# Performance work log

Measured on AMD Instinct MI355X. Metric: run time of the kernel, lower is better.

## Reference

```python
import jax, jax.numpy as jnp
import numpy as np

K = 8  # hardcoded knn_point(8, ...) in the original module


def setup_inputs() -> dict:
    key = jax.random.key(0)
    k1, k2, k3 = jax.random.split(key, 3)
    B, N, S, C = 8, 8192, 2048, 256
    return {
        "xyz": jax.random.normal(k1, (B, 3, N), dtype=jnp.float32),
        "sparse_xyz": jax.random.normal(k2, (B, 3, S), dtype=jnp.float32),
        "sparse_feat": jax.random.normal(k3, (B, C, S), dtype=jnp.float32),
    }


def reference(xyz, sparse_xyz, sparse_feat):
    # xyz: [B,3,N] dense query points; sparse_xyz: [B,3,S]; sparse_feat: [B,C,S]
    B, _, N = xyz.shape
    x = jnp.transpose(xyz, (0, 2, 1))          # [B,N,3]
    sx = jnp.transpose(sparse_xyz, (0, 2, 1))  # [B,S,3]
    sf = jnp.transpose(sparse_feat, (0, 2, 1)) # [B,S,C]

    sqr = (jnp.sum(x * x, axis=-1)[:, :, None]
           + jnp.sum(sx * sx, axis=-1)[:, None, :]
           - 2.0 * jnp.einsum('bnc,bsc->bns', x, sx))

    # K nearest neighbors (smallest distance) -> indices [B,N,K]
    _, idx = jax.lax.top_k(-sqr, K)

    bidx = jnp.arange(B)[:, None, None]
    g_xyz = sx[bidx, idx]                      # gather neighbor coords [B,N,K,3]
    diff = g_xyz - x[:, :, None, :]
    dist = jnp.maximum(jnp.linalg.norm(diff, axis=3), 1e-10)  # [B,N,K]

    inv = 1.0 / dist
    weight = inv / jnp.sum(inv, axis=2, keepdims=True)        # [B,N,K]

    g_feat = sf[bidx, idx]                     # gather neighbor feats [B,N,K,C]
    dense = jnp.sum(weight[..., None] * g_feat, axis=2)       # [B,N,C]
    return jnp.transpose(dense, (0, 2, 1))     # [B,C,N]
```

## Files before the change

### kernel.cpp

```cpp
#include <hip/hip_runtime.h>
#include <hip/hip_fp16.h>

#define BB 8
#define NN 8192
#define SS 2048
#define CC 256
#define KNN 8
#define TOPM 10
#define NLIST 4
#define QPB 64
#define MSTRIDE 41
#define FSTR 12

#define UMIN(a, b) __builtin_elementwise_min(a, b)
#define UMAX(a, b) __builtin_elementwise_max(a, b)
#define UMIN3(a, b, c) UMIN(UMIN(a, b), c)

typedef short bf16x8_t __attribute__((ext_vector_type(8)));
typedef float f32x4_t __attribute__((ext_vector_type(4)));

__device__ __forceinline__ unsigned pack_h2(float a, float b) {
    __half2 h = __halves2half2(__float2half_rn(a), __float2half_rn(b));
    return *reinterpret_cast<unsigned*>(&h);
}
__device__ __forceinline__ float2 unpack_h2(unsigned u) {
    __half2 h = *reinterpret_cast<__half2*>(&u);
    return __half22float2(h);
}

__device__ __forceinline__ unsigned short f2bf(float f) {
    unsigned u = __float_as_uint(f);
    u += 0x7FFFu + ((u >> 16) & 1u);
    return (unsigned short)(u >> 16);
}
__device__ __forceinline__ float bf2f(unsigned short h) {
    return __uint_as_float((unsigned)h << 16);
}

__device__ __forceinline__ void ins2(unsigned k1[TOPM], unsigned ca, unsigned cb) {
    unsigned lo = UMIN(ca, cb), hi = UMAX(ca, cb);
#pragma unroll
    for (int j = TOPM - 1; j >= 2; --j)
        k1[j] = UMIN3(k1[j], UMAX(k1[j - 1], lo), UMAX(k1[j - 2], hi));
    k1[1] = UMIN3(k1[1], UMAX(k1[0], lo), hi);
    k1[0] = UMIN(k1[0], lo);
}

__device__ __forceinline__ void ins_step(unsigned k1[TOPM], f32x4_t d, unsigned sbase) {
    unsigned c0 = (__float_as_uint(d[0]) & 0xFFFFF800u) | sbase;
    unsigned c1 = (__float_as_uint(d[1]) & 0xFFFFF800u) | (sbase + 1u);
    unsigned c2 = (__float_as_uint(d[2]) & 0xFFFFF800u) | (sbase + 2u);
    unsigned c3 = (__float_as_uint(d[3]) & 0xFFFFF800u) | (sbase + 3u);
    ins2(k1, c0, c1);
    ins2(k1, c2, c3);
}

__global__ __launch_bounds__(256) void prep_kernel(
    const float* __restrict__ sxyz,
    unsigned short* __restrict__ gt)
{
    const int b = blockIdx.x;
    const int tid = threadIdx.x;
    const float* sb = sxyz + (long)b * 3 * SS;
    unsigned short* gb = gt + (long)b * 2 * SS * 8;
#pragma unroll
    for (int i = 0; i < SS / 256; ++i) {
        int s = i * 256 + tid;
        float px = sb[s], py = sb[SS + s], pz = sb[2 * SS + s];
        unsigned short xh = f2bf(px); unsigned short xl = f2bf(px - bf2f(xh));
        unsigned short yh = f2bf(py); unsigned short yl = f2bf(py - bf2f(yh));
        unsigned short zh = f2bf(pz); unsigned short zl = f2bf(pz - bf2f(zh));
        float pn = fmaf(px, px, fmaf(py, py, pz * pz));
        unsigned short nh = f2bf(pn); unsigned short nl = f2bf(pn - bf2f(nh));
        const unsigned ONE = 0x3F80u;
        uint4 t0 = make_uint4((unsigned)xh | ((unsigned)xl << 16),
                              (unsigned)xh | ((unsigned)yh << 16),
                              (unsigned)yl | ((unsigned)yh << 16),
                              (unsigned)zh | ((unsigned)zl << 16));
        uint4 t1 = make_uint4((unsigned)zh | ((unsigned)nh << 16),
                              (unsigned)nl | (ONE << 16),
                              ONE, 0u);
        *(uint4*)&gb[(long)s * 8] = t0;
        *(uint4*)&gb[((long)SS + s) * 8] = t1;
    }
}

__global__ __launch_bounds__(256, 4) void knn_kernel(
    const float* __restrict__ xyz,
    const float* __restrict__ sxyz,
    const unsigned short* __restrict__ gt,
    unsigned* __restrict__ out_pk)
{
    __shared__ unsigned mbuf[QPB * MSTRIDE];

    const int b    = blockIdx.x >> 7;
    const int q0   = (blockIdx.x & 127) * QPB;
    const int tid  = threadIdx.x;
    const int wave = tid >> 6;
    const int lane = tid & 63;
    const int g    = lane >> 4;
    const int qi   = lane & 15;

    const float* sb = sxyz + (long)b * 3 * SS;
    const float* xb = xyz + (long)b * 3 * NN;

    const int nq = q0 + wave * 16 + qi;
    const float qx = xb[nq], qy = xb[NN + nq], qz = xb[2 * NN + nq];

    bf16x8_t qf = (bf16x8_t)0;
    {
        unsigned short xh = f2bf(qx); float xhf = bf2f(xh);
        unsigned short yh = f2bf(qy); float yhf = bf2f(yh);
        unsigned short zh = f2bf(qz); float zhf = bf2f(zh);
        unsigned short xh2 = f2bf(-2.f * xhf), xl2 = f2bf(-2.f * (qx - xhf));
        unsigned short yh2 = f2bf(-2.f * yhf), yl2 = f2bf(-2.f * (qy - yhf));
        unsigned short zh2 = f2bf(-2.f * zhf), zl2 = f2bf(-2.f * (qz - zhf));
        float qn = fmaf(qx, qx, fmaf(qy, qy, qz * qz)) + 0.0625f;
        unsigned short nh = f2bf(qn); unsigned short nl = f2bf(qn - bf2f(nh));
        const short ONE = (short)0x3F80;
        if (g == 0) {
            qf[0] = (short)xh2; qf[1] = (short)xh2; qf[2] = (short)xl2;
            qf[3] = (short)yh2; qf[4] = (short)yh2; qf[5] = (short)yl2;
            qf[6] = (short)zh2; qf[7] = (short)zh2;
        } else if (g == 1) {
            qf[0] = (short)zl2; qf[1] = ONE; qf[2] = ONE;
            qf[3] = (short)nh;  qf[4] = (short)nl;
        }
    }

    const unsigned short* abase =
        gt + (long)b * 2 * SS * 8 + (long)(g & 1) * SS * 8 + qi * 8;

    unsigned k1[TOPM];
#pragma unroll
    for (int j = 0; j < TOPM; ++j) k1[j] = 0xFFFFFFFFu;

    const f32x4_t zacc = {0.f, 0.f, 0.f, 0.f};
    const unsigned ib4 = (unsigned)(g * 4);

    bf16x8_t af = *(const bf16x8_t*)abase; abase += 128;
    f32x4_t dc = __builtin_amdgcn_mfma_f32_16x16x32_bf16(af, qf, zacc, 0, 0, 0);

#pragma unroll 2
    for (int step = 0; step < 127; ++step) {
        bf16x8_t an = *(const bf16x8_t*)abase; abase += 128;
        f32x4_t dn = __builtin_amdgcn_mfma_f32_16x16x32_bf16(an, qf, zacc, 0, 0, 0);
        ins_step(k1, dc, ib4 + (unsigned)(step * 16));
        dc = dn;
    }
    ins_step(k1, dc, ib4 + (unsigned)(127 * 16));

    {
        unsigned* m1 = &mbuf[(wave * 16 + qi) * MSTRIDE + g * TOPM];
#pragma unroll
        for (int j = 0; j < TOPM; ++j) m1[j] = k1[j];
    }
    __syncthreads();

    if (tid < QPB) {
        const int n2 = q0 + tid;
        const double dqx = (double)xb[n2], dqy = (double)xb[NN + n2], dqz = (double)xb[2 * NN + n2];
        const unsigned* ml = &mbuf[tid * MSTRIDE];

        unsigned long long top[KNN];
#pragma unroll
        for (int j = 0; j < KNN; ++j) top[j] = ~0ull;

#pragma unroll 4
        for (int j = 0; j < NLIST * TOPM; ++j) {
            unsigned key = ml[j];
            int s = key & 0x7FF;
            float px = sb[s], py = sb[SS + s], pz = sb[2 * SS + s];
            double ex = (double)px - dqx;
            double ey = (double)py - dqy;
            double ez = (double)pz - dqz;
            double dd = ex * ex + ey * ey + ez * ez;
            unsigned long long c =
                (((unsigned long long)__double_as_longlong(dd)) & ~0x7FFull) | (unsigned long long)s;
#pragma unroll
            for (int jj = KNN - 1; jj >= 1; --jj)
                top[jj] = UMIN(UMAX(top[jj - 1], c), top[jj]);
            top[0] = UMIN(top[0], c);
        }

        const float fqx = xb[n2], fqy = xb[NN + n2], fqz = xb[2 * NN + n2];
        int   id[KNN];
        float inv[KNN];
        float ssum = 0.f;
#pragma unroll
        for (int k = 0; k < KNN; ++k) {
            id[k] = (int)(top[k] & 0x7FFull);
            float px = sb[id[k]], py = sb[SS + id[k]], pz = sb[2 * SS + id[k]];
            float dx = px - fqx, dy = py - fqy, dz = pz - fqz;
            float dv = sqrtf(dx * dx + dy * dy + dz * dz);
            dv = fmaxf(dv, 1e-10f);
            inv[k] = 1.0f / dv;
            ssum += inv[k];
        }
        const float rs = 1.0f / ssum;
        const long base = ((long)b * NN + n2) * KNN;
#pragma unroll
        for (int k = 0; k < KNN; ++k) {
            unsigned hw = (unsigned)__half_as_ushort(__float2half_rn(inv[k] * rs));
            out_pk[base + k] = (hw << 16) | (unsigned)id[k];
        }
    }
}

__global__ __launch_bounds__(256, 2) void accum_kernel(
    const float*    __restrict__ sf,
    const unsigned* __restrict__ pk,
    float* __restrict__ out)
{
    __shared__ unsigned short feat[SS * FSTR];

    const int blk  = blockIdx.x;
    const int b    = blk >> 6;
    const int ct   = (blk >> 1) & 31;
    const int half = blk & 1;
    const int t    = threadIdx.x;
    const int c0   = ct * 8;

    const float* sfb = sf + ((long)b * CC + c0) * SS;
#pragma unroll
    for (int i = 0; i < SS / 256; ++i) {
        int s = i * 256 + t;
        float f[8];
#pragma unroll
        for (int c = 0; c < 8; ++c) f[c] = sfb[(long)c * SS + s];
        uint2 w0 = make_uint2(pack_h2(f[0], f[1]), pack_h2(f[2], f[3]));
        uint2 w1 = make_uint2(pack_h2(f[4], f[5]), pack_h2(f[6], f[7]));
        *(uint2*)&feat[s * FSTR]     = w0;
        *(uint2*)&feat[s * FSTR + 4] = w1;
    }
    __syncthreads();

    const unsigned* pkb = pk + ((long)b * NN + half * 4096) * KNN;
    float* outb = out + ((long)b * CC + c0) * NN + half * 4096;

    for (int it = 0; it < 4096 / 256; ++it) {
        const int nrel = it * 256 + t;
        const uint4 pa = *(const uint4*)(pkb + (long)nrel * KNN);
        const uint4 pb = *(const uint4*)(pkb + (long)nrel * KNN + 4);
        const unsigned pks[8] = {pa.x, pa.y, pa.z, pa.w, pb.x, pb.y, pb.z, pb.w};

        float acc[8];
#pragma unroll
        for (int c = 0; c < 8; ++c) acc[c] = 0.f;

#pragma unroll
        for (int k = 0; k < KNN; ++k) {
            const unsigned p = pks[k];
            const int id = p & 0x7FF;
            const float w = __half2float(__ushort_as_half((unsigned short)(p >> 16)));
            const unsigned short* fp = &feat[id * FSTR];
            uint2 A = *(const uint2*)fp;
            uint2 B = *(const uint2*)(fp + 4);
            float2 f0 = unpack_h2(A.x), f1 = unpack_h2(A.y);
            float2 f2 = unpack_h2(B.x), f3 = unpack_h2(B.y);
            acc[0] = fmaf(w, f0.x, acc[0]);
            acc[1] = fmaf(w, f0.y, acc[1]);
            acc[2] = fmaf(w, f1.x, acc[2]);
            acc[3] = fmaf(w, f1.y, acc[3]);
            acc[4] = fmaf(w, f2.x, acc[4]);
            acc[5] = fmaf(w, f2.y, acc[5]);
            acc[6] = fmaf(w, f3.x, acc[6]);
            acc[7] = fmaf(w, f3.y, acc[7]);
        }

#pragma unroll
        for (int c = 0; c < 8; ++c)
            outb[(long)c * NN + nrel] = acc[c];
    }
}

extern "C" void kernel_launch(void* const* d_in, const int* in_sizes, int n_in,
                              void* d_out, int out_size, void* d_ws, size_t ws_size,
                              hipStream_t stream) {
    const float* xyz  = (const float*)d_in[0];
    const float* sxyz = (const float*)d_in[1];
    const float* sf   = (const float*)d_in[2];
    float* out = (float*)d_out;

    unsigned* pkbuf = (unsigned*)d_ws;
    unsigned short* gtile = (unsigned short*)((char*)d_ws + (size_t)BB * NN * KNN * 4);

    prep_kernel<<<dim3(BB), dim3(256), 0, stream>>>(sxyz, gtile);
    knn_kernel<<<dim3(BB * NN / QPB), dim3(256), 0, stream>>>(xyz, sxyz, gtile, pkbuf);
    accum_kernel<<<dim3(BB * 32 * 2), dim3(256), 0, stream>>>(sf, pkbuf, out);
}
```

Baseline: 175.6 us.

## Fuse feature accumulation into knn kernel using pre-transposed fp16 features

Adds a prep kernel that transposes sparse features into an [B,S,C] fp16 layout. The weighted gather-accumulate is folded into the knn kernel: neighbor indices and weights stay in LDS, and each block reads 16-byte feature rows from global/L2 instead of staging 8-channel slices in LDS. This drops the packed-index workspace round trip and the separate accum launch. In exchange, feature gathers become scattered global reads. Output stores also become strided, with four threads per query writing channels NN apart, so store coalescing worsens.

Result: slower. 179.3 us (+2.1%).

```diff
diff --git a/kernel.cpp b/kernel.cpp
--- a/kernel.cpp
+++ b/kernel.cpp
@@ -10,7 +10,7 @@
 #define NLIST 4
 #define QPB 64
 #define MSTRIDE 41
-#define FSTR 12
+#define TSTR 264
 
 #define UMIN(a, b) __builtin_elementwise_min(a, b)
 #define UMAX(a, b) __builtin_elementwise_max(a, b)
@@ -19,10 +19,6 @@
 typedef short bf16x8_t __attribute__((ext_vector_type(8)));
 typedef float f32x4_t __attribute__((ext_vector_type(4)));
 
-__device__ __forceinline__ unsigned pack_h2(float a, float b) {
-    __half2 h = __halves2half2(__float2half_rn(a), __float2half_rn(b));
-    return *reinterpret_cast<unsigned*>(&h);
-}
 __device__ __forceinline__ float2 unpack_h2(unsigned u) {
     __half2 h = *reinterpret_cast<__half2*>(&u);
     return __half22float2(h);
@@ -85,13 +81,46 @@
     }
 }
 
+__global__ __launch_bounds__(256) void prep2_kernel(
+    const float* __restrict__ sf,
+    unsigned short* __restrict__ sft)
+{
+    __shared__ unsigned short ts[64 * TSTR];
+
+    const int blk = blockIdx.x;
+    const int b   = blk >> 5;
+    const int st  = blk & 31;
+    const int t   = threadIdx.x;
+
+    const int s  = t & 63;
+    const int cq = t >> 6;
+    const float* sfb = sf + (long)b * CC * SS + (long)st * 64;
+#pragma unroll
+    for (int it = 0; it < CC / 4; ++it) {
+        int c = it * 4 + cq;
+        float v = sfb[(long)c * SS + s];
+        ts[s * TSTR + c] = __half_as_ushort(__float2half_rn(v));
+    }
+    __syncthreads();
+
+    const int so = t >> 2;
+    const int co = (t & 3) * 64;
+    unsigned short* dst = sft + ((long)b * SS + st * 64 + so) * CC + co;
+    const unsigned short* src = &ts[so * TSTR + co];
+#pragma unroll
+    for (int i = 0; i < 8; ++i)
+        *(uint4*)&dst[i * 8] = *(const uint4*)&src[i * 8];
+}
+
 __global__ __launch_bounds__(256, 4) void knn_kernel(
     const float* __restrict__ xyz,
     const float* __restrict__ sxyz,
     const unsigned short* __restrict__ gt,
-    unsigned* __restrict__ out_pk)
+    const unsigned short* __restrict__ sft,
+    float* __restrict__ out)
 {
     __shared__ unsigned mbuf[QPB * MSTRIDE];
+    __shared__ unsigned pk_lds[QPB * KNN];
 
     const int b    = blockIdx.x >> 7;
     const int q0   = (blockIdx.x & 127) * QPB;
@@ -128,7 +157,7 @@
         }
     }
 
-    const unsigned short* abase =
+    const unsigned short* ap =
         gt + (long)b * 2 * SS * 8 + (long)(g & 1) * SS * 8 + qi * 8;
 
     unsigned k1[TOPM];
@@ -138,12 +167,12 @@
     const f32x4_t zacc = {0.f, 0.f, 0.f, 0.f};
     const unsigned ib4 = (unsigned)(g * 4);
 
-    bf16x8_t af = *(const bf16x8_t*)abase; abase += 128;
+    bf16x8_t af = *(const bf16x8_t*)ap; ap += 128;
     f32x4_t dc = __builtin_amdgcn_mfma_f32_16x16x32_bf16(af, qf, zacc, 0, 0, 0);
 
 #pragma unroll 2
     for (int step = 0; step < 127; ++step) {
-        bf16x8_t an = *(const bf16x8_t*)abase; abase += 128;
+        bf16x8_t an = *(const bf16x8_t*)ap; ap += 128;
         f32x4_t dn = __builtin_amdgcn_mfma_f32_16x16x32_bf16(an, qf, zacc, 0, 0, 0);
         ins_step(k1, dc, ib4 + (unsigned)(step * 16));
         dc = dn;
@@ -198,79 +227,52 @@
             ssum += inv[k];
         }
         const float rs = 1.0f / ssum;
-        const long base = ((long)b * NN + n2) * KNN;
 #pragma unroll
         for (int k = 0; k < KNN; ++k) {
             unsigned hw = (unsigned)__half_as_ushort(__float2half_rn(inv[k] * rs));
-            out_pk[base + k] = (hw << 16) | (unsigned)id[k];
-        }
-    }
-}
-
-__global__ __launch_bounds__(256, 2) void accum_kernel(
-    const float*    __restrict__ sf,
-    const unsigned* __restrict__ pk,
-    float* __restrict__ out)
-{
-    __shared__ unsigned short feat[SS * FSTR];
-
-    const int blk  = blockIdx.x;
-    const int b    = blk >> 6;
-    const int ct   = (blk >> 1) & 31;
-    const int half = blk & 1;
-    const int t    = threadIdx.x;
-    const int c0   = ct * 8;
-
-    const float* sfb = sf + ((long)b * CC + c0) * SS;
-#pragma unroll
-    for (int i = 0; i < SS / 256; ++i) {
-        int s = i * 256 + t;
-        float f[8];
-#pragma unroll
-        for (int c = 0; c < 8; ++c) f[c] = sfb[(long)c * SS + s];
-        uint2 w0 = make_uint2(pack_h2(f[0], f[1]), pack_h2(f[2], f[3]));
-        uint2 w1 = make_uint2(pack_h2(f[4], f[5]), pack_h2(f[6], f[7]));
-        *(uint2*)&feat[s * FSTR]     = w0;
-        *(uint2*)&feat[s * FSTR + 4] = w1;
+            pk_lds[tid * KNN + k] = (hw << 16) | (unsigned)id[k];
+        }
     }
     __syncthreads();
 
-    const unsigned* pkb = pk + ((long)b * NN + half * 4096) * KNN;
-    float* outb = out + ((long)b * CC + c0) * NN + half * 4096;
-
-    for (int it = 0; it < 4096 / 256; ++it) {
-        const int nrel = it * 256 + t;
-        const uint4 pa = *(const uint4*)(pkb + (long)nrel * KNN);
-        const uint4 pb = *(const uint4*)(pkb + (long)nrel * KNN + 4);
-        const unsigned pks[8] = {pa.x, pa.y, pa.z, pa.w, pb.x, pb.y, pb.z, pb.w};
-
-        float acc[8];
-#pragma unroll
-        for (int c = 0; c < 8; ++c) acc[c] = 0.f;
-
-#pragma unroll
-        for (int k = 0; k < KNN; ++k) {
-            const unsigned p = pks[k];
-            const int id = p & 0x7FF;
-            const float w = __half2float(__ushort_as_half((unsigned short)(p >> 16)));
-            const unsigned short* fp = &feat[id * FSTR];
-            uint2 A = *(const uint2*)fp;
-            uint2 B = *(const uint2*)(fp + 4);
-            float2 f0 = unpack_h2(A.x), f1 = unpack_h2(A.y);
-            float2 f2 = unpack_h2(B.x), f3 = unpack_h2(B.y);
-            acc[0] = fmaf(w, f0.x, acc[0]);
-            acc[1] = fmaf(w, f0.y, acc[1]);
-            acc[2] = fmaf(w, f1.x, acc[2]);
-            acc[3] = fmaf(w, f1.y, acc[3]);
-            acc[4] = fmaf(w, f2.x, acc[4]);
-            acc[5] = fmaf(w, f2.y, acc[5]);
-            acc[6] = fmaf(w, f3.x, acc[6]);
-            acc[7] = fmaf(w, f3.y, acc[7]);
-        }
-
-#pragma unroll
-        for (int c = 0; c < 8; ++c)
-            outb[(long)c * NN + nrel] = acc[c];
+    {
+        const int q  = tid >> 2;
+        const int cl = tid & 3;
+        const unsigned short* sfb = sft + (long)b * SS * CC;
+        float* outq = out + (long)b * CC * NN + (q0 + q);
+
+        unsigned pks[KNN];
+#pragma unroll
+        for (int k = 0; k < KNN; ++k) pks[k] = pk_lds[q * KNN + k];
+
+#pragma unroll
+        for (int cc = 0; cc < 8; ++cc) {
+            const int ch = cc * 32 + cl * 8;
+            float acc[8];
+#pragma unroll
+            for (int j = 0; j < 8; ++j) acc[j] = 0.f;
+
+#pragma unroll
+            for (int k = 0; k < KNN; ++k) {
+                const unsigned p = pks[k];
+                const int idp = p & 0x7FF;
+                const float w = __half2float(__ushort_as_half((unsigned short)(p >> 16)));
+                const uint4 F = *(const uint4*)&sfb[(long)idp * CC + ch];
+                float2 f0 = unpack_h2(F.x), f1 = unpack_h2(F.y);
+                float2 f2 = unpack_h2(F.z), f3 = unpack_h2(F.w);
+                acc[0] = fmaf(w, f0.x, acc[0]);
+                acc[1] = fmaf(w, f0.y, acc[1]);
+                acc[2] = fmaf(w, f1.x, acc[2]);
+                acc[3] = fmaf(w, f1.y, acc[3]);
+                acc[4] = fmaf(w, f2.x, acc[4]);
+                acc[5] = fmaf(w, f2.y, acc[5]);
+                acc[6] = fmaf(w, f3.x, acc[6]);
+                acc[7] = fmaf(w, f3.y, acc[7]);
+            }
+#pragma unroll
+            for (int j = 0; j < 8; ++j)
+                outq[(long)(ch + j) * NN] = acc[j];
+        }
     }
 }
 
@@ -282,10 +284,10 @@
     const float* sf   = (const float*)d_in[2];
     float* out = (float*)d_out;
 
-    unsigned* pkbuf = (unsigned*)d_ws;
-    unsigned short* gtile = (unsigned short*)((char*)d_ws + (size_t)BB * NN * KNN * 4);
+    unsigned short* gtile = (unsigned short*)d_ws;
+    unsigned short* sft   = (unsigned short*)((char*)d_ws + 512 * 1024);
 
     prep_kernel<<<dim3(BB), dim3(256), 0, stream>>>(sxyz, gtile);
-    knn_kernel<<<dim3(BB * NN / QPB), dim3(256), 0, stream>>>(xyz, sxyz, gtile, pkbuf);
-    accum_kernel<<<dim3(BB * 32 * 2), dim3(256), 0, stream>>>(sf, pkbuf, out);
-}
+    prep2_kernel<<<dim3(BB * 32), dim3(256), 0, stream>>>(sf, sft);
+    knn_kernel<<<dim3(BB * NN / QPB), dim3(256), 0, stream>>>(xyz, sxyz, gtile, sft, out);
+}
```
